# Optimization experiments

Hardware: AMD Instinct MI355X
Metric: run time of the kernel (lower is better)

## Reference

```python
import math
import jax, jax.numpy as jnp
import numpy as np

N_WL = 262144
T_REF = 273.15          # CONSTANTS.STANDARD_TEMPERATURE [K]
P_REF = 101325.0        # CONSTANTS.STANDARD_PRESSURE [Pa]
C_LIGHT = 2.99792458e8  # CONSTANTS.SPEED_OF_LIGHT
K_B = 1.380649e-23      # CONSTANTS.BOLTZMANN
N_AVO = 6.02214076e23   # CONSTANTS.AVOGADRO

# hard-coded line database: [center_wl, strength, width, temp_exp]; rows 0-2 O3, 3-5 H2O, 6-9 CO2
LINES = np.array([
    [254.0, 1.15e-17, 2.0, 0.05], [280.0, 5e-18, 3.0, 0.04], [310.0, 1.9e-19, 2.5, 0.03],
    [940.0, 2.5e-23, 3.0, 0.4],  [1130.0, 8.2e-24, 2.5, 0.35], [1380.0, 1.8e-22, 4.0, 0.45],
    [1400.0, 3.5e-25, 3.0, 0.5], [1600.0, 7.8e-26, 2.5, 0.48], [2000.0, 4.2e-24, 4.0, 0.52],
    [2700.0, 1.2e-24, 3.5, 0.49]], dtype=np.float32)
MASS = np.array([48.0]*3 + [18.0]*3 + [44.0]*4, dtype=np.float32)


def setup_inputs() -> dict:
    key = jax.random.key(0)
    ks = jax.random.split(key, 8)
    inp = {
        'wavelengths': jnp.linspace(200.0, 3000.0, N_WL, dtype=jnp.float32),
        'temperature': jnp.float32(250.0),
        'pressure': jnp.float32(80000.0),
        'conc_o3': jnp.float32(1e-6),
        'conc_h2o': jnp.float32(1e-2),
        'conc_co2': jnp.float32(4e-4),
        'mix_w1': jax.random.normal(ks[0], (10, 64), jnp.float32) * 0.3,
        'mix_b1': jnp.zeros((64,), jnp.float32),
        'mix_w2': jax.random.normal(ks[1], (64, 64), jnp.float32) * 0.12,
        'mix_b2': jnp.zeros((64,), jnp.float32),
        'mix_w3': jax.random.normal(ks[2], (64, N_WL), jnp.float32) * 0.12,
        'mix_b3': jnp.zeros((N_WL,), jnp.float32),
        'cont_w1': jax.random.normal(ks[3], (5, 32), jnp.float32) * 0.4,
        'cont_b1': jnp.zeros((32,), jnp.float32),
        'cont_w2': jax.random.normal(ks[4], (32, N_WL), jnp.float32) * 0.17,
        'cont_b2': jnp.zeros((N_WL,), jnp.float32),
    }
    return inp


def _voigt(wl, nu0, gamma_L, gamma_D):
    # wl: [N]; nu0, gamma_L, gamma_D: [L] -> returns [L, N]
    sigma = gamma_D / (math.sqrt(2.0 * math.log(2.0)) + 1e-12)          # [L]
    x = (wl[None, :] - nu0[:, None]) / (sigma[:, None] + 1e-12)          # [L,N]
    y = (gamma_L / (sigma + 1e-12))[:, None]                             # [L,1]
    t = y - 1j * x
    s = jnp.abs(x) + y
    mask1 = s >= 15.0
    mask2 = (s < 15.0) & (jnp.abs(x) >= 5.5)
    w1 = (t * 0.5641896 / (0.5 + t ** 2)).real
    u = t ** 2
    w2 = (t * (1.410474 + u * 0.5641896) / (0.75 + u * (3.0 + u))).real
    w3 = (jnp.exp(-x ** 2) * jnp.cos(2.0 * x * y) / math.sqrt(math.pi)
          + 2.0 * y / math.pi * jnp.sin(x ** 2) / (x ** 2 + y ** 2 + 1e-10))
    result = jnp.where(mask1, w1, jnp.where(mask2, w2, w3))
    return result / (sigma[:, None] * math.sqrt(math.pi) + 1e-12)


def reference(wavelengths, temperature, pressure, conc_o3, conc_h2o, conc_co2,
              mix_w1, mix_b1, mix_w2, mix_b2, mix_w3, mix_b3,
              cont_w1, cont_b1, cont_w2, cont_b2):
    lines = jnp.asarray(LINES)
    mass = jnp.asarray(MASS)
    conc = jnp.stack([conc_o3, conc_o3, conc_o3,
                      conc_h2o, conc_h2o, conc_h2o,
                      conc_co2, conc_co2, conc_co2, conc_co2])          # [10]
    nu0, strength, width, temp_exp = lines[:, 0], lines[:, 1], lines[:, 2], lines[:, 3]
    strength_T = strength * (T_REF / (temperature + 1e-12)) ** temp_exp  # [10]
    gamma_L = width * (pressure / (P_REF + 1e-12)) * jnp.sqrt(T_REF / (temperature + 1e-12))
    gamma_D = nu0 / C_LIGHT * jnp.sqrt(2.0 * K_B * temperature * N_AVO / (mass + 1e-12))

    profiles = _voigt(wavelengths, nu0, gamma_L, gamma_D)                # [10,N]
    cross = jnp.sum((conc * strength_T)[:, None] * profiles, axis=0)     # [N]

    # continuum net: 5 -> 32 (SiLU) -> N (softplus)
    cont_feat = jnp.stack([temperature / (T_REF + 1e-12),
                           pressure / (P_REF + 1e-12),
                           conc_h2o,
                           jnp.float32(1.0), jnp.float32(0.0)])
    h = jax.nn.silu(cont_feat @ cont_w1 + cont_b1)
    continuum = jax.nn.softplus(h @ cont_w2 + cont_b2)
    cross = cross + continuum

    # line-mixing net: 10 -> 64 (SiLU) -> 64 (SiLU) -> N (sigmoid); dropout is eval-mode identity
    mix_feat = jnp.concatenate([jnp.stack([temperature / (T_REF + 1e-12),
                                           pressure / (P_REF + 1e-12)]),
                                cross[:8]])
    m = jax.nn.silu(mix_feat @ mix_w1 + mix_b1)
    m = jax.nn.silu(m @ mix_w2 + mix_b2)
    mixing = jax.nn.sigmoid(m @ mix_w3 + mix_b3)
    return cross * (1.0 + 0.1 * (mixing - 0.5))
```

## Files before the change

### kernel.cpp

```cpp
#include <hip/hip_runtime.h>
#include <math.h>

#define N_WL 262144

#define T_REF 273.15
#define P_REF 101325.0
#define C_LIGHT 299792458.0
#define K_B 1.380649e-23
#define N_AVO 6.02214076e+23

__constant__ float c_nu0[10]  = {254.0f, 280.0f, 310.0f, 940.0f, 1130.0f, 1380.0f, 1400.0f, 1600.0f, 2000.0f, 2700.0f};
__constant__ float c_str[10]  = {1.15e-17f, 5e-18f, 1.9e-19f, 2.5e-23f, 8.2e-24f, 1.8e-22f, 3.5e-25f, 7.8e-26f, 4.2e-24f, 1.2e-24f};
__constant__ float c_wid[10]  = {2.0f, 3.0f, 2.5f, 3.0f, 2.5f, 4.0f, 3.0f, 2.5f, 4.0f, 3.5f};
__constant__ float c_texp[10] = {0.05f, 0.04f, 0.03f, 0.4f, 0.35f, 0.45f, 0.5f, 0.48f, 0.52f, 0.49f};
__constant__ float c_mass[10] = {48.f, 48.f, 48.f, 18.f, 18.f, 18.f, 44.f, 44.f, 44.f, 44.f};
__constant__ int   c_cidx[10] = {0, 0, 0, 1, 1, 1, 2, 2, 2, 2};

#define WS_M2    0
#define WS_H     64
#define WS_NU0   96
#define WS_ISIG  106
#define WS_Y     116
#define WS_SCALE 126
#define WS_TOT   136

__device__ __forceinline__ float siluf(float x)     { return x / (1.0f + __expf(-x)); }
__device__ __forceinline__ float sigmoidf(float x)  { return 1.0f / (1.0f + __expf(-x)); }
__device__ __forceinline__ float softplusf(float x) { return fmaxf(x, 0.0f) + log1pf(expf(-fabsf(x))); }

__device__ __forceinline__ float voigt_w(float x, float y) {
    float ax = fabsf(x);
    float s  = ax + y;
    if (s >= 15.0f) {
        float ur = y * y - x * x;
        float ui = -2.0f * x * y;
        float dr = 0.5f + ur, di = ui;
        float nr = 0.5641896f * y, ni = 0.5641896f * (-x);
        float den = dr * dr + di * di;
        return (nr * dr + ni * di) / den;
    } else if (ax >= 5.5f) {
        float ur = y * y - x * x;
        float ui = -2.0f * x * y;
        float pr = 1.410474f + 0.5641896f * ur;
        float pi_ = 0.5641896f * ui;
        float tr = y, ti = -x;
        float nr = tr * pr - ti * pi_;
        float ni = tr * pi_ + ti * pr;
        float u2r = ur * ur - ui * ui;
        float u2i = 2.0f * ur * ui;
        float dr = 0.75f + 3.0f * ur + u2r;
        float di = 3.0f * ui + u2i;
        float den = dr * dr + di * di;
        return (nr * dr + ni * di) / den;
    } else {
        float x2 = x * x;
        return expf(-x2) * cosf(2.0f * x * y) * 0.5641895835477563f
             + (2.0f * y / 3.14159265358979f) * sinf(x2) / (x2 + y * y + 1e-10f);
    }
}

__global__ void GasAbs_setup_kernel(
    const float* __restrict__ wl,
    const float* __restrict__ Tp, const float* __restrict__ Pp,
    const float* __restrict__ o3, const float* __restrict__ h2o, const float* __restrict__ co2,
    const float* __restrict__ mix_w1, const float* __restrict__ mix_b1,
    const float* __restrict__ mix_w2, const float* __restrict__ mix_b2,
    const float* __restrict__ cont_w1, const float* __restrict__ cont_b1,
    const float* __restrict__ cont_w2, const float* __restrict__ cont_b2,
    float* __restrict__ ws)
{
    __shared__ float sp[WS_TOT];
    __shared__ float s_feat[10];
    __shared__ float s_m1[64];

    const int t = threadIdx.x;
    const double T = (double)Tp[0];
    const double P = (double)Pp[0];
    const float  cc[3] = {o3[0], h2o[0], co2[0]};

    if (t < 10) {
        double nu0 = (double)c_nu0[t];
        double sT  = (double)c_str[t] * pow(T_REF / (T + 1e-12), (double)c_texp[t]);
        double gL  = (double)c_wid[t] * (P / (P_REF + 1e-12)) * sqrt(T_REF / (T + 1e-12));
        double gD  = nu0 / C_LIGHT * sqrt(2.0 * K_B * T * N_AVO / ((double)c_mass[t] + 1e-12));
        double sig = gD / (sqrt(2.0 * log(2.0)) + 1e-12);
        sp[WS_NU0  + t] = (float)nu0;
        sp[WS_ISIG + t] = (float)(1.0 / (sig + 1e-12));
        sp[WS_Y    + t] = (float)(gL / (sig + 1e-12));
        sp[WS_SCALE+ t] = (float)((double)cc[c_cidx[t]] * sT / (sig * sqrt(M_PI) + 1e-12));
    }
    if (t < 32) {
        float cf[5];
        cf[0] = (float)(T / (T_REF + 1e-12));
        cf[1] = (float)(P / (P_REF + 1e-12));
        cf[2] = cc[1];
        cf[3] = 1.0f;
        cf[4] = 0.0f;
        float a = cont_b1[t];
        #pragma unroll
        for (int k = 0; k < 5; k++) a += cf[k] * cont_w1[k * 32 + t];
        sp[WS_H + t] = siluf(a);
    }
    __syncthreads();

    if (t < 8) {
        float w = wl[t];
        float c = cont_b2[t];
        #pragma unroll
        for (int j = 0; j < 32; j++) c += sp[WS_H + j] * cont_w2[(size_t)j * N_WL + t];
        float cross = softplusf(c);
        #pragma unroll
        for (int l = 0; l < 10; l++) {
            float x = (w - sp[WS_NU0 + l]) * sp[WS_ISIG + l];
            cross += sp[WS_SCALE + l] * voigt_w(x, sp[WS_Y + l]);
        }
        s_feat[2 + t] = cross;
    }
    if (t == 0) {
        s_feat[0] = (float)(T / (T_REF + 1e-12));
        s_feat[1] = (float)(P / (P_REF + 1e-12));
    }
    __syncthreads();

    {
        float a = mix_b1[t];
        #pragma unroll
        for (int k = 0; k < 10; k++) a += s_feat[k] * mix_w1[k * 64 + t];
        s_m1[t] = siluf(a);
    }
    __syncthreads();

    {
        float a = mix_b2[t];
        #pragma unroll
        for (int k = 0; k < 64; k++) a += s_m1[k] * mix_w2[k * 64 + t];
        sp[WS_M2 + t] = siluf(a);
    }
    __syncthreads();

    ws[t] = sp[t];
    if (t < WS_TOT - 64) ws[64 + t] = sp[64 + t];
}

__global__ __launch_bounds__(256) void GasAbs_main_kernel(
    const float* __restrict__ wl,
    const float* __restrict__ mix_w3, const float* __restrict__ mix_b3,
    const float* __restrict__ cont_w2, const float* __restrict__ cont_b2,
    const float* __restrict__ ws,
    float* __restrict__ out)
{
    __shared__ float sp[WS_TOT];
    const int t = threadIdx.x;
    if (t < WS_TOT) sp[t] = ws[t];
    __syncthreads();

    const int i = blockIdx.x * 256 + t;

    const float w = wl[i];

    float c = cont_b2[i];
    #pragma unroll
    for (int j = 0; j < 32; j++)
        c = fmaf(sp[WS_H + j], cont_w2[(size_t)j * N_WL + i], c);

    float cross = softplusf(c);

    #pragma unroll
    for (int l = 0; l < 10; l++) {
        const float x = (w - sp[WS_NU0 + l]) * sp[WS_ISIG + l];
        cross = fmaf(sp[WS_SCALE + l], voigt_w(x, sp[WS_Y + l]), cross);
    }

    float m = mix_b3[i];
    #pragma unroll
    for (int j = 0; j < 64; j++)
        m = fmaf(sp[WS_M2 + j], mix_w3[(size_t)j * N_WL + i], m);

    out[i] = cross * (0.95f + 0.1f * sigmoidf(m));
}

extern "C" void kernel_launch(void* const* d_in, const int* in_sizes, int n_in,
                              void* d_out, int out_size, void* d_ws, size_t ws_size,
                              hipStream_t stream) {
    const float* wl      = (const float*)d_in[0];
    const float* Tp      = (const float*)d_in[1];
    const float* Pp      = (const float*)d_in[2];
    const float* o3      = (const float*)d_in[3];
    const float* h2o     = (const float*)d_in[4];
    const float* co2     = (const float*)d_in[5];
    const float* mix_w1  = (const float*)d_in[6];
    const float* mix_b1  = (const float*)d_in[7];
    const float* mix_w2  = (const float*)d_in[8];
    const float* mix_b2  = (const float*)d_in[9];
    const float* mix_w3  = (const float*)d_in[10];
    const float* mix_b3  = (const float*)d_in[11];
    const float* cont_w1 = (const float*)d_in[12];
    const float* cont_b1 = (const float*)d_in[13];
    const float* cont_w2 = (const float*)d_in[14];
    const float* cont_b2 = (const float*)d_in[15];
    float* ws  = (float*)d_ws;
    float* out = (float*)d_out;

    GasAbs_setup_kernel<<<1, 64, 0, stream>>>(
        wl, Tp, Pp, o3, h2o, co2,
        mix_w1, mix_b1, mix_w2, mix_b2,
        cont_w1, cont_b1, cont_w2, cont_b2, ws);

    const int threads = 256;
    const int blocks  = N_WL / threads;
    GasAbs_main_kernel<<<blocks, threads, 0, stream>>>(
        wl, mix_w3, mix_b3, cont_w2, cont_b2, ws, out);
}
```

Baseline: 152.7 us.

## Split each output element's reductions across two half-wavefronts and combine via shuffle

Each 64-lane wavefront now handles 32 output elements. The two 32-lane halves each take half of the continuum dot product, half of the mixing dot product and half of the Voigt lines, and the partial sums are combined with cross-lane xor shuffles. The grid doubles so there are twice as many threads in flight, aimed at hiding memory latency on the strided weight reads. In exchange, each global load now covers only 32 contiguous floats (128 bytes) instead of 256 bytes per wavefront, and the final softplus, sigmoid and store run on only half the lanes. Launch bounds also request 8 blocks per multiprocessor.

After: 156.8 us. 2.7% more time.

```diff
diff --git a/kernel.cpp b/kernel.cpp
--- a/kernel.cpp
+++ b/kernel.cpp
@@ -142,7 +142,7 @@
     if (t < WS_TOT - 64) ws[64 + t] = sp[64 + t];
 }
 
-__global__ __launch_bounds__(256) void GasAbs_main_kernel(
+__global__ __launch_bounds__(256, 8) void GasAbs_main_kernel(
     const float* __restrict__ wl,
     const float* __restrict__ mix_w3, const float* __restrict__ mix_b3,
     const float* __restrict__ cont_w2, const float* __restrict__ cont_b2,
@@ -154,29 +154,47 @@
     if (t < WS_TOT) sp[t] = ws[t];
     __syncthreads();
 
-    const int i = blockIdx.x * 256 + t;
+    const int lane = t & 63;
+    const int half = lane >> 5;
+    const int eidx = lane & 31;
+    const int i = blockIdx.x * 128 + (t >> 6) * 32 + eidx;
 
     const float w = wl[i];
 
-    float c = cont_b2[i];
-    #pragma unroll
-    for (int j = 0; j < 32; j++)
-        c = fmaf(sp[WS_H + j], cont_w2[(size_t)j * N_WL + i], c);
-
-    float cross = softplusf(c);
-
-    #pragma unroll
-    for (int l = 0; l < 10; l++) {
-        const float x = (w - sp[WS_NU0 + l]) * sp[WS_ISIG + l];
-        cross = fmaf(sp[WS_SCALE + l], voigt_w(x, sp[WS_Y + l]), cross);
-    }
-
-    float m = mix_b3[i];
-    #pragma unroll
-    for (int j = 0; j < 64; j++)
-        m = fmaf(sp[WS_M2 + j], mix_w3[(size_t)j * N_WL + i], m);
-
-    out[i] = cross * (0.95f + 0.1f * sigmoidf(m));
+    float c = (half == 0) ? cont_b2[i] : 0.0f;
+    {
+        const int j0 = half * 16;
+        #pragma unroll
+        for (int j = 0; j < 16; j++)
+            c = fmaf(sp[WS_H + j0 + j], cont_w2[(size_t)(j0 + j) * N_WL + i], c);
+    }
+
+    float v = 0.0f;
+    {
+        const int l0 = half * 5;
+        #pragma unroll
+        for (int l = 0; l < 5; l++) {
+            const float x = (w - sp[WS_NU0 + l0 + l]) * sp[WS_ISIG + l0 + l];
+            v = fmaf(sp[WS_SCALE + l0 + l], voigt_w(x, sp[WS_Y + l0 + l]), v);
+        }
+    }
+
+    float m = (half == 1) ? mix_b3[i] : 0.0f;
+    {
+        const int j0 = half * 32;
+        #pragma unroll
+        for (int j = 0; j < 32; j++)
+            m = fmaf(sp[WS_M2 + j0 + j], mix_w3[(size_t)(j0 + j) * N_WL + i], m);
+    }
+
+    const float c_tot = c + __shfl_xor(c, 32, 64);
+    const float v_tot = v + __shfl_xor(v, 32, 64);
+    const float m_tot = m + __shfl_xor(m, 32, 64);
+
+    if (half == 0) {
+        const float cross = softplusf(c_tot) + v_tot;
+        out[i] = cross * (0.95f + 0.1f * sigmoidf(m_tot));
+    }
 }
 
 extern "C" void kernel_launch(void* const* d_in, const int* in_sizes, int n_in,
@@ -207,7 +225,7 @@
         cont_w1, cont_b1, cont_w2, cont_b2, ws);
 
     const int threads = 256;
-    const int blocks  = N_WL / threads;
+    const int blocks  = N_WL / 128;
     GasAbs_main_kernel<<<blocks, threads, 0, stream>>>(
         wl, mix_w3, mix_b3, cont_w2, cont_b2, ws, out);
 }
```
